# Kernel tuning notes

Measured on AMD Instinct MI355X. Metric: run time of the kernel, lower is better.

## Reference

```python
import jax, jax.numpy as jnp
import numpy as np

N, IN_DIM, HID, TASK, L = 4096, 256, 256, 128, 2
NEG_INF = -9e15


def setup_inputs() -> dict:
    key = jax.random.key(0)
    ks = jax.random.split(key, 16)
    s = 0.02
    return {
        "h": jax.random.normal(ks[0], (N, IN_DIM), jnp.float32),
        "adj": jax.random.randint(ks[1], (N, N), 0, 2, jnp.int32),
        "z": jax.random.normal(ks[2], (N, TASK), jnp.float32),
        # initial projection (in_dim -> hidden)
        "Wp": jax.random.normal(ks[3], (IN_DIM, HID), jnp.float32) * s,
        "bp": jnp.zeros((HID,), jnp.float32),
        # per-layer params, stacked over L layers
        "Wm": jax.random.normal(ks[4], (L, HID, HID), jnp.float32) * s,
        "bm": jnp.zeros((L, HID), jnp.float32),
        "Wg": jax.random.normal(ks[5], (L, HID + TASK, HID), jnp.float32) * s,
        "bg": jnp.zeros((L, HID), jnp.float32),
        "Wk": jax.random.normal(ks[6], (L, HID, HID), jnp.float32) * s,
        "bk": jnp.zeros((L, HID), jnp.float32),
        "Wq": jax.random.normal(ks[7], (L, HID, HID), jnp.float32) * s,
        "bq": jnp.zeros((L, HID), jnp.float32),
        # attention vector a: [L, 2*out_dim]; first half pairs with k, second with q
        "a": jax.random.normal(ks[8], (L, 2 * HID), jnp.float32),
    }


def reference(h, adj, z, Wp, bp, Wm, bm, Wg, bg, Wk, bk, Wq, bq, a):
    mask = adj > 0  # [N, N]
    h = h @ Wp + bp  # initial_proj -> [N, HID]
    n_layers = Wm.shape[0]
    total_gate_l1 = jnp.float32(0.0)
    for l in range(n_layers):
        raw_message = jax.nn.relu(h @ Wm[l] + bm[l])  # [N, d]
        gate = jax.nn.sigmoid(jnp.concatenate([h, z], axis=1) @ Wg[l] + bg[l])
        gated_message = gate * raw_message
        total_gate_l1 = total_gate_l1 + jnp.sum(jnp.abs(gate)) / gate.size
        q = gated_message @ Wq[l] + bq[l]  # [N, d]
        k = h @ Wk[l] + bk[l]              # [N, d]
        d = q.shape[1]
        # e[i, j] = leaky_relu([k_j, q_i] @ a) = leaky_relu(k_j . a[:d] + q_i . a[d:])
        kk = k @ a[l, :d]  # [N]
        qq = q @ a[l, d:]  # [N]
        e = jax.nn.leaky_relu(qq[:, None] + kk[None, :])  # [N, N], slope 0.01 matches torch
        attention = jax.nn.softmax(jnp.where(mask, e, NEG_INF), axis=1)
        agg_message = attention.T @ gated_message  # [N, d]
        h = (agg_message + h) / 2
    return h, total_gate_l1 / n_layers
```

## Files before the change

kernel.cpp:

```cpp
#include <hip/hip_runtime.h>
#include <hip/hip_bf16.h>
#include <stdint.h>

static constexpr int cN    = 4096;
static constexpr int cHID  = 256;
static constexpr int cTASK = 128;
static constexpr int cL    = 2;
static constexpr float RLN2 = 1.4426950408889634f;

typedef short bf16x8 __attribute__((ext_vector_type(8)));
typedef float f32x4  __attribute__((ext_vector_type(4)));

#define MFMA(a, b, c) __builtin_amdgcn_mfma_f32_16x16x32_bf16((a), (b), (c), 0, 0, 0)

static __device__ __forceinline__ uint16_t f2bf(float f) {
    uint32_t u = __float_as_uint(f);
    uint32_t r = (u + 0x7FFFu + ((u >> 16) & 1u)) >> 16;
    return (uint16_t)r;
}
static __device__ __forceinline__ float bf2f(uint16_t h) {
    return __uint_as_float(((uint32_t)h) << 16);
}
static __device__ __forceinline__ bf16x8 ld_frag(const uint16_t* p) {
    return *reinterpret_cast<const bf16x8*>(p);
}
static __device__ __forceinline__ uint32_t pkf16(float a, float b) {
    _Float16 ha = (_Float16)a, hb = (_Float16)b;
    uint16_t ua, ub;
    __builtin_memcpy(&ua, &ha, 2);
    __builtin_memcpy(&ub, &hb, 2);
    return (uint32_t)ua | ((uint32_t)ub << 16);
}
static __device__ __forceinline__ float f16lo(uint32_t v) {
    uint16_t u = (uint16_t)(v & 0xFFFFu); _Float16 h;
    __builtin_memcpy(&h, &u, 2); return (float)h;
}
static __device__ __forceinline__ float f16hi(uint32_t v) {
    uint16_t u = (uint16_t)(v >> 16); _Float16 h;
    __builtin_memcpy(&h, &u, 2); return (float)h;
}
static __device__ __forceinline__ uint32_t spread4(uint32_t x) {
    x = (x | (x << 12)) & 0x000F000Fu;
    x = (x | (x << 6))  & 0x03030303u;
    x = (x | (x << 3))  & 0x11111111u;
    return x;
}
static __device__ __forceinline__ void gload_lds16(const void* g, void* l) {
    __builtin_amdgcn_global_load_lds((const __attribute__((address_space(1))) void*)g,
                                     (__attribute__((address_space(3))) void*)l, 16, 0, 0);
}

static __device__ __forceinline__ void castT_body(const float* __restrict__ S,
                                                  uint16_t* __restrict__ D, int K, int bx,
                                                  uint16_t (*t)[72]) {
    int ntk = K / 64;
    int tk = (bx % ntk) * 64;
    int td = (bx / ntk) * 64;
    int lane = threadIdx.x & 63, w = threadIdx.x >> 6;
    for (int r = w; r < 64; r += 4) t[r][lane] = f2bf(S[(size_t)(tk + r) * 256 + td + lane]);
    __syncthreads();
    for (int r = w; r < 64; r += 4) D[(size_t)(td + r) * K + tk + lane] = t[lane][r];
}

__global__ __launch_bounds__(256) void k_prep(const float* __restrict__ h,
                                              const float* __restrict__ z,
                                              const float* __restrict__ Wp,
                                              const float* __restrict__ Wm,
                                              const float* __restrict__ Wg,
                                              const float* __restrict__ Wq,
                                              const float* __restrict__ bq,
                                              const float* __restrict__ Wk,
                                              const float* __restrict__ bk,
                                              const float* __restrict__ a,
                                              const int* __restrict__ adj,
                                              uint16_t* __restrict__ hin_bf,
                                              uint16_t* __restrict__ z_bf,
                                              uint16_t* __restrict__ WpT,
                                              uint16_t* __restrict__ WmT,
                                              uint16_t* __restrict__ WgT,
                                              float* __restrict__ wqv,
                                              float* __restrict__ wkv,
                                              float* __restrict__ cvec,
                                              uint32_t* __restrict__ maskw,
                                              float* __restrict__ gsum) {
    __shared__ uint16_t sht[64][72];
    __shared__ float shf[2][256];
    int b = blockIdx.x, tid = threadIdx.x;
    if (b == 0 && tid == 0) gsum[0] = 0.f;
    if (b < 1024) {
        int idx = b * 256 + tid;
        float4 v = reinterpret_cast<const float4*>(h)[idx];
        ushort4 o; o.x = f2bf(v.x); o.y = f2bf(v.y); o.z = f2bf(v.z); o.w = f2bf(v.w);
        reinterpret_cast<ushort4*>(hin_bf)[idx] = o;
        return;
    }
    b -= 1024;
    if (b < 512) {
        int idx = b * 256 + tid;
        float4 v = reinterpret_cast<const float4*>(z)[idx];
        ushort4 o; o.x = f2bf(v.x); o.y = f2bf(v.y); o.z = f2bf(v.z); o.w = f2bf(v.w);
        reinterpret_cast<ushort4*>(z_bf)[idx] = o;
        return;
    }
    b -= 512;
    if (b < 16) { castT_body(Wp, WpT, 256, b, sht); return; }
    b -= 16;
    if (b < 32) { castT_body(Wm + (b >> 4) * 65536, WmT + (b >> 4) * 65536, 256, b & 15, sht); return; }
    b -= 32;
    if (b < 48) { castT_body(Wg + (b / 24) * 98304, WgT + (b / 24) * 98304, 384, b % 24, sht); return; }
    b -= 48;
    if (b < 16) {
        int l = b >> 3, which = (b >> 2) & 1, q = b & 3;
        int lane = tid & 63, wid = tid >> 6;
        const float* W    = which ? (Wk + l * 65536) : (Wq + l * 65536);
        const float* avec = a + l * 512 + (which ? 0 : 256);
        float* av = shf[0];
        float* red = shf[1];
        av[tid] = avec[tid];
        __syncthreads();
        float av0 = av[lane], av1 = av[64 + lane], av2 = av[128 + lane], av3 = av[192 + lane];
        float* wv = which ? wkv : wqv;
        for (int dd = 0; dd < 16; ++dd) {
            int d = q * 64 + wid * 16 + dd;
            const float* Wr = W + (size_t)d * 256;
            float s = Wr[lane] * av0 + Wr[64 + lane] * av1 + Wr[128 + lane] * av2 + Wr[192 + lane] * av3;
            for (int off = 32; off; off >>= 1) s += __shfl_down(s, off, 64);
            if (lane == 0) wv[l * 256 + d] = s * RLN2;
        }
        if (q == 0) {
            const float* bias = which ? (bk + l * 256) : (bq + l * 256);
            red[tid] = bias[tid] * av[tid];
            __syncthreads();
            for (int off = 128; off; off >>= 1) {
                if (tid < off) red[tid] += red[tid + off];
                __syncthreads();
            }
            if (tid == 0) cvec[l * 2 + which] = red[0] * RLN2;
        }
        return;
    }
    b -= 16;
    {
        int wid = tid >> 6, lane = tid & 63;
        int i = b * 4 + wid;
        const int* row = adj + (size_t)i * cN;
        uint32_t* orow = maskw + (size_t)i * 128;
        for (int ch = 0; ch < 16; ++ch) {
            int4 v = reinterpret_cast<const int4*>(row + ch * 256)[lane];
            uint64_t b0 = __ballot(v.x > 0);
            uint64_t b1 = __ballot(v.y > 0);
            uint64_t b2 = __ballot(v.z > 0);
            uint64_t b3 = __ballot(v.w > 0);
            int k = lane & 7;
            uint32_t e0 = spread4((uint32_t)(b0 >> (8 * k)) & 0xFFu);
            uint32_t e1 = spread4((uint32_t)(b1 >> (8 * k)) & 0xFFu);
            uint32_t e2 = spread4((uint32_t)(b2 >> (8 * k)) & 0xFFu);
            uint32_t e3 = spread4((uint32_t)(b3 >> (8 * k)) & 0xFFu);
            if (lane < 8) orow[ch * 8 + k] = e0 | (e1 << 1) | (e2 << 2) | (e3 << 3);
        }
    }
}

__global__ __launch_bounds__(256) void k_pt(const uint32_t* __restrict__ maskw,
                                            uint32_t* __restrict__ maskT,
                                            const uint16_t* __restrict__ hin_bf,
                                            const uint16_t* __restrict__ WpT,
                                            const float* __restrict__ bp,
                                            float* __restrict__ h_f32,
                                            uint16_t* __restrict__ hcur_bf) {
    __shared__ uint32_t ml[256][9];
    int tid = threadIdx.x;
    if (blockIdx.x < 256) {
        int bi = blockIdx.x & 15, bj = blockIdx.x >> 4;
        int i0 = bi * 256, j0 = bj * 256;
        {
            const uint32_t* src = maskw + (size_t)(i0 + tid) * 128 + bj * 8;
            uint4 a = *reinterpret_cast<const uint4*>(src);
            uint4 b = *reinterpret_cast<const uint4*>(src + 4);
            ml[tid][0] = a.x; ml[tid][1] = a.y; ml[tid][2] = a.z; ml[tid][3] = a.w;
            ml[tid][4] = b.x; ml[tid][5] = b.y; ml[tid][6] = b.z; ml[tid][7] = b.w;
        }
        __syncthreads();
        int lane = tid & 63, wid = tid >> 6;
        int tw = wid * 2 + (lane >> 5);
        int l31 = lane & 31;
        uint32_t ow[8];
#pragma unroll
        for (int ti = 0; ti < 8; ++ti) {
            uint32_t m = ml[ti * 32 + l31][tw];
            uint32_t myw = 0;
#pragma unroll
            for (int c = 0; c < 32; ++c) {
                uint64_t bl = __ballot(((m >> c) & 1) != 0);
                uint32_t v = (lane < 32) ? (uint32_t)bl : (uint32_t)(bl >> 32);
                if (l31 == c) myw = v;
            }
            ow[ti] = myw;
        }
        uint32_t* dst = maskT + (size_t)(j0 + tw * 32 + l31) * 128 + bi * 8;
        *reinterpret_cast<uint4*>(dst)     = make_uint4(ow[0], ow[1], ow[2], ow[3]);
        *reinterpret_cast<uint4*>(dst + 4) = make_uint4(ow[4], ow[5], ow[6], ow[7]);
        return;
    }
    int bb = blockIdx.x - 256;
    int bx = bb & 63, by = bb >> 6;
    int lane = tid & 63, wid = tid >> 6;
    int wr = wid >> 1, wc = wid & 1;
    int l16 = lane & 15, g = lane >> 4;
    int i0 = bx * 64 + wr * 32, d0 = by * 64 + wc * 32;
    f32x4 acc[2][2] = {};
#pragma unroll
    for (int ks = 0; ks < 8; ++ks) {
        int kb = ks * 32 + g * 8;
        bf16x8 afr[2], bfr[2];
#pragma unroll
        for (int mr = 0; mr < 2; ++mr) afr[mr] = ld_frag(hin_bf + (size_t)(i0 + mr * 16 + l16) * 256 + kb);
#pragma unroll
        for (int nr = 0; nr < 2; ++nr) bfr[nr] = ld_frag(WpT + (size_t)(d0 + nr * 16 + l16) * 256 + kb);
#pragma unroll
        for (int mr = 0; mr < 2; ++mr)
#pragma unroll
            for (int nr = 0; nr < 2; ++nr)
                acc[mr][nr] = MFMA(afr[mr], bfr[nr], acc[mr][nr]);
    }
#pragma unroll
    for (int mr = 0; mr < 2; ++mr)
#pragma unroll
        for (int nr = 0; nr < 2; ++nr) {
            int d = d0 + nr * 16 + l16;
            float bias = bp[d];
#pragma unroll
            for (int r = 0; r < 4; ++r) {
                int i = i0 + mr * 16 + g * 4 + r;
                float v = acc[mr][nr][r] + bias;
                h_f32[(size_t)i * 256 + d] = v;
                hcur_bf[(size_t)i * 256 + d] = f2bf(v);
            }
        }
}

__global__ __launch_bounds__(256) void k_msgg(const uint16_t* __restrict__ hcur_bf,
                                              const uint16_t* __restrict__ z_bf,
                                              const uint16_t* __restrict__ WmT,
                                              const uint16_t* __restrict__ WgT,
                                              const float* __restrict__ bm,
                                              const float* __restrict__ bg,
                                              const float* __restrict__ wqv,
                                              const float* __restrict__ wkv,
                                              const float* __restrict__ cvec,
                                              uint16_t* __restrict__ gmT,
                                              float* __restrict__ qqp,
                                              float* __restrict__ kkv,
                                              float* __restrict__ gsum,
                                              int layer) {
    __shared__ float wkv_s[256], wqv_s[256];
    __shared__ float wred[4];
    int tid = threadIdx.x;
    wkv_s[tid] = wkv[layer * 256 + tid];
    wqv_s[tid] = wqv[layer * 256 + tid];
    __syncthreads();

    int bx = blockIdx.x, by = blockIdx.y;
    int lane = tid & 63, wid = tid >> 6;
    int wr = wid >> 1, wc = wid & 1;
    int l16 = lane & 15, g = lane >> 4;
    int i0 = bx * 64 + wr * 32, d0 = by * 64 + wc * 32;
    bool doKK = (by == 0);
    const uint16_t* WmTl = WmT + layer * 65536;
    const uint16_t* WgTl = WgT + layer * 98304;
    f32x4 am[2][2] = {}, ag[2][2] = {};
    float kkp[2] = {0.f, 0.f};
#pragma unroll
    for (int ks = 0; ks < 8; ++ks) {
        int kb = ks * 32 + g * 8;
        bf16x8 afr[2], bmf[2], bgf[2];
#pragma unroll
        for (int mr = 0; mr < 2; ++mr) afr[mr] = ld_frag(hcur_bf + (size_t)(i0 + mr * 16 + l16) * 256 + kb);
#pragma unroll
        for (int nr = 0; nr < 2; ++nr) {
            bmf[nr] = ld_frag(WmTl + (size_t)(d0 + nr * 16 + l16) * 256 + kb);
            bgf[nr] = ld_frag(WgTl + (size_t)(d0 + nr * 16 + l16) * 384 + kb);
        }
        if (doKK) {
#pragma unroll
            for (int mr = 0; mr < 2; ++mr)
#pragma unroll
                for (int u = 0; u < 8; ++u)
                    kkp[mr] += bf2f((uint16_t)afr[mr][u]) * wkv_s[kb + u];
        }
#pragma unroll
        for (int mr = 0; mr < 2; ++mr)
#pragma unroll
            for (int nr = 0; nr < 2; ++nr) {
                am[mr][nr] = MFMA(afr[mr], bmf[nr], am[mr][nr]);
                ag[mr][nr] = MFMA(afr[mr], bgf[nr], ag[mr][nr]);
            }
    }
#pragma unroll
    for (int ks = 0; ks < 4; ++ks) {
        int kb = ks * 32 + g * 8;
        bf16x8 afr[2], bgf[2];
#pragma unroll
        for (int mr = 0; mr < 2; ++mr) afr[mr] = ld_frag(z_bf + (size_t)(i0 + mr * 16 + l16) * 128 + kb);
#pragma unroll
        for (int nr = 0; nr < 2; ++nr) bgf[nr] = ld_frag(WgTl + (size_t)(d0 + nr * 16 + l16) * 384 + 256 + kb);
#pragma unroll
        for (int mr = 0; mr < 2; ++mr)
#pragma unroll
            for (int nr = 0; nr < 2; ++nr)
                ag[mr][nr] = MFMA(afr[mr], bgf[nr], ag[mr][nr]);
    }
    float gs = 0.f;
    float qqt[2][4] = {};
#pragma unroll
    for (int mr = 0; mr < 2; ++mr)
#pragma unroll
        for (int nr = 0; nr < 2; ++nr) {
            int d = d0 + nr * 16 + l16;
            float bmv = bm[layer * 256 + d], bgv = bg[layer * 256 + d];
            float wqd = wqv_s[d];
            ushort4 pack;
#pragma unroll
            for (int r = 0; r < 4; ++r) {
                float rm = am[mr][nr][r] + bmv; rm = rm > 0.f ? rm : 0.f;
                float gt = 1.f / (1.f + __expf(-(ag[mr][nr][r] + bgv)));
                gs += gt;
                float gmv = gt * rm;
                qqt[mr][r] += gmv * wqd;
                ((uint16_t*)&pack)[r] = f2bf(gmv);
            }
            int i = i0 + mr * 16 + g * 4;
            *reinterpret_cast<ushort4*>(gmT + (size_t)d * cN + i) = pack;
        }
#pragma unroll
    for (int mr = 0; mr < 2; ++mr)
#pragma unroll
        for (int r = 0; r < 4; ++r) {
            float v = qqt[mr][r];
            v += __shfl_xor(v, 1, 64);
            v += __shfl_xor(v, 2, 64);
            v += __shfl_xor(v, 4, 64);
            v += __shfl_xor(v, 8, 64);
            if (l16 == 0) qqp[(size_t)(by * 2 + wc) * cN + i0 + mr * 16 + g * 4 + r] = v;
        }
    if (doKK) {
        float cc = cvec[layer * 2 + 0] + cvec[layer * 2 + 1];
#pragma unroll
        for (int mr = 0; mr < 2; ++mr) {
            float v = kkp[mr];
            v += __shfl_xor(v, 16, 64);
            v += __shfl_xor(v, 32, 64);
            if (lane < 16) kkv[i0 + mr * 16 + l16] = v + cc;
        }
    }
    for (int off = 32; off; off >>= 1) gs += __shfl_down(gs, off, 64);
    if (lane == 0) wred[wid] = gs;
    __syncthreads();
    if (tid == 0) atomicAdd(gsum, wred[0] + wred[1] + wred[2] + wred[3]);
}

__global__ __launch_bounds__(256) void k_stats(const float* __restrict__ qqp,
                                               const float* __restrict__ kkv,
                                               const uint32_t* __restrict__ maskw,
                                               float2* __restrict__ stats2) {
    int wid = threadIdx.x >> 6, lane = threadIdx.x & 63;
    int i = blockIdx.x * 4 + wid;
    float qq = 0.f;
#pragma unroll
    for (int s = 0; s < 8; ++s) qq += qqp[(size_t)s * cN + i];
    const uint32_t* mrow = maskw + (size_t)i * 128;
    float den = 0.f;
#pragma unroll 4
    for (int c = 0; c < 64; ++c) {
        int j = c * 64 + lane;
        uint32_t w = mrow[j >> 5];
        bool on = (w >> (j & 31)) & 1;
        float e = qq + kkv[j];
        e = fmaxf(e, 0.01f * e);
        e = fminf(e, 80.f);
        den += on ? exp2f(e) : 0.f;
    }
#pragma unroll
    for (int off = 32; off; off >>= 1) den += __shfl_xor(den, off, 64);
    if (lane == 0) stats2[i] = make_float2(qq, den > 0.f ? 1.f / den : 0.f);
}

__global__ __launch_bounds__(512, 4) void k_agg(const uint16_t* __restrict__ gmT,
                                                const float2* __restrict__ stats2,
                                                const uint32_t* __restrict__ maskT,
                                                const float* __restrict__ kkv,
                                                uint32_t* __restrict__ part) {
    __shared__ uint16_t B_lds[2][256 * 64];
    __shared__ uint16_t A_lds[2][64 * 64];
    int jb = blockIdx.x, seg = blockIdx.y;
    int tid = threadIdx.x, lane = tid & 63, wid = tid >> 6;
    int l16 = lane & 15, g = lane >> 4;
    int jg = wid >> 2, dg = wid & 3;
    int jt = jb * 64;
    int ib0 = seg * 512;
    f32x4 acc[2][4] = {};

    int io8 = 8 * ((lane & 7) ^ (lane >> 3));
    const uint16_t* gsrc0 = gmT + (size_t)(wid * 32 + (lane >> 3)) * cN + ib0 + io8;
    auto stageB = [&](int buf, int stg) {
        const uint16_t* gs = gsrc0 + stg * 64;
        uint16_t* ldst = &B_lds[buf][(wid * 32) * 64];
#pragma unroll
        for (int c = 0; c < 4; ++c)
            gload_lds16(gs + (size_t)(c * 8) * cN, ldst + (c * 8) * 64);
    };
    int at_j = tid >> 3, at_io = tid & 7;
    float kk_t = kkv[jt + at_j];
    const uint32_t* mrow_t = maskT + (size_t)(jt + at_j) * 128;
    int ash = (at_io * 16) ^ ((at_j & 7) << 4);
    uint8_t* arow[2] = { reinterpret_cast<uint8_t*>(&A_lds[0][0]) + at_j * 128 + ash,
                         reinterpret_cast<uint8_t*>(&A_lds[1][0]) + at_j * 128 + ash };
    auto stageA = [&](int buf, int stg) {
        int ib = ib0 + stg * 64 + at_io * 8;
        uint32_t mword = mrow_t[ib >> 5];
        int shift = ib & 31;
        const float2* sp = stats2 + ib;
        union { bf16x8 v; uint16_t s[8]; } aw;
#pragma unroll
        for (int u = 0; u < 8; ++u) {
            float2 st = sp[u];
            float e = st.x + kk_t;
            e = fmaxf(e, 0.01f * e);
            e = fminf(e, 80.f);
            float w = exp2f(e) * st.y;
            aw.s[u] = ((mword >> (shift + u)) & 1) ? f2bf(w) : (uint16_t)0;
        }
        *reinterpret_cast<bf16x8*>(arow[buf]) = aw.v;
    };

    stageB(0, 0);
    stageA(0, 0);
    __syncthreads();
    int rxor = (l16 & 7) << 4;

    for (int stg = 0; stg < 8; ++stg) {
        if (stg < 7) {
            stageB((stg + 1) & 1, stg + 1);
            stageA((stg + 1) & 1, stg + 1);
        }
        const uint8_t* cb = reinterpret_cast<const uint8_t*>(&B_lds[stg & 1][0]);
        const uint8_t* ca = reinterpret_cast<const uint8_t*>(&A_lds[stg & 1][0]);
#pragma unroll
        for (int k = 0; k < 2; ++k) {
            int cofs = (k * 64 + g * 16);
            bf16x8 a0 = *reinterpret_cast<const bf16x8*>(ca + (size_t)(jg * 32 + l16) * 128 + (cofs ^ rxor));
            bf16x8 a1 = *reinterpret_cast<const bf16x8*>(ca + (size_t)(jg * 32 + 16 + l16) * 128 + (cofs ^ rxor));
            const uint8_t* bcol = cb + (size_t)(dg * 64 + l16) * 128 + (cofs ^ rxor);
#pragma unroll
            for (int nf = 0; nf < 4; ++nf) {
                bf16x8 bfr = *reinterpret_cast<const bf16x8*>(bcol + nf * (16 * 128));
                acc[0][nf] = MFMA(a0, bfr, acc[0][nf]);
                acc[1][nf] = MFMA(a1, bfr, acc[1][nf]);
            }
        }
        __syncthreads();
    }
    uint32_t* pb = part + ((size_t)(seg * 64 + jb) * 8 + wid) * 1024;
#pragma unroll
    for (int mf = 0; mf < 2; ++mf)
#pragma unroll
        for (int nf = 0; nf < 4; ++nf)
#pragma unroll
            for (int rr = 0; rr < 2; ++rr)
                pb[(((mf * 4 + nf) * 2) + rr) * 64 + lane] =
                    pkf16(acc[mf][nf][rr * 2], acc[mf][nf][rr * 2 + 1]);
}

__global__ __launch_bounds__(256) void k_resid(const uint32_t* __restrict__ part,
                                               float* __restrict__ h_f32,
                                               uint16_t* __restrict__ hcur_bf,
                                               float* __restrict__ out,
                                               const float* __restrict__ gsum,
                                               int last) {
    int jb = blockIdx.x >> 3, wid = blockIdx.x & 7;
    int tid = threadIdx.x;
    int jg = wid >> 2, dg = wid & 3;
    if (last && blockIdx.x == 0 && tid == 0)
        out[(size_t)cN * cHID] = gsum[0] * (1.f / ((float)(cN * cHID) * (float)cL));
    const uint32_t* pb = part + ((size_t)jb * 8 + wid) * 1024;
#pragma unroll
    for (int t = 0; t < 4; ++t) {
        int idx = t * 256 + tid;
        float s0 = 0.f, s1 = 0.f;
#pragma unroll
        for (int seg = 0; seg < 8; ++seg) {
            uint32_t v = pb[(size_t)seg * (64 * 8 * 1024) + idx];
            s0 += f16lo(v); s1 += f16hi(v);
        }
        int mf = idx >> 9, nf = (idx >> 7) & 3, rr = (idx >> 6) & 1, lane = idx & 63;
        int j = jb * 64 + jg * 32 + mf * 16 + (lane >> 4) * 4 + rr * 2;
        int d = dg * 64 + nf * 16 + (lane & 15);
        size_t i0 = (size_t)j * 256 + d, i1 = i0 + 256;
        float v0 = (s0 + h_f32[i0]) * 0.5f;
        float v1 = (s1 + h_f32[i1]) * 0.5f;
        if (last) {
            out[i0] = v0; out[i1] = v1;
        } else {
            h_f32[i0] = v0; h_f32[i1] = v1;
            hcur_bf[i0] = f2bf(v0); hcur_bf[i1] = f2bf(v1);
        }
    }
}

extern "C" void kernel_launch(void* const* d_in, const int* in_sizes, int n_in,
                              void* d_out, int out_size, void* d_ws, size_t ws_size,
                              hipStream_t stream) {
    const float* h   = (const float*)d_in[0];
    const int*   adj = (const int*)d_in[1];
    const float* z   = (const float*)d_in[2];
    const float* Wp  = (const float*)d_in[3];
    const float* bp  = (const float*)d_in[4];
    const float* Wm  = (const float*)d_in[5];
    const float* bm  = (const float*)d_in[6];
    const float* Wg  = (const float*)d_in[7];
    const float* bg  = (const float*)d_in[8];
    const float* Wk  = (const float*)d_in[9];
    const float* bk  = (const float*)d_in[10];
    const float* Wq  = (const float*)d_in[11];
    const float* bq  = (const float*)d_in[12];
    const float* a   = (const float*)d_in[13];
    float* out = (float*)d_out;

    uint8_t* ws = (uint8_t*)d_ws;
    size_t cur = 0;
    auto alloc = [&](size_t bytes) -> uint8_t* {
        uint8_t* p = ws + cur;
        cur = (cur + bytes + 255) & ~(size_t)255;
        return p;
    };
    uint32_t* maskw  = (uint32_t*)alloc((size_t)cN * 128 * 4);
    uint32_t* maskT  = (uint32_t*)alloc((size_t)cN * 128 * 4);
    float*    h_f32  = (float*)   alloc((size_t)cN * 256 * 4);
    uint16_t* hin_bf = (uint16_t*)alloc((size_t)cN * 256 * 2);
    uint16_t* hcur   = (uint16_t*)alloc((size_t)cN * 256 * 2);
    uint16_t* z_bf   = (uint16_t*)alloc((size_t)cN * 128 * 2);
    uint16_t* WpT    = (uint16_t*)alloc(65536 * 2);
    uint16_t* WmT    = (uint16_t*)alloc((size_t)cL * 65536 * 2);
    uint16_t* WgT    = (uint16_t*)alloc((size_t)cL * 98304 * 2);
    uint16_t* gmT    = (uint16_t*)alloc((size_t)cN * 256 * 2);
    float*    wqv    = (float*)   alloc(cL * 256 * 4);
    float*    wkv    = (float*)   alloc(cL * 256 * 4);
    float*    cvec   = (float*)   alloc(256);
    float*    qqp    = (float*)   alloc(8ull * cN * 4);
    float*    kk     = (float*)   alloc(cN * 4);
    float2*   stats2 = (float2*)  alloc(cN * 8);
    float*    gsum   = (float*)   alloc(256);
    uint32_t* part   = (uint32_t*)alloc(8ull * cN * 256 * 2);
    (void)cur;

    k_prep<<<2672, 256, 0, stream>>>(h, z, Wp, Wm, Wg, Wq, bq, Wk, bk, a, adj,
                                     hin_bf, z_bf, WpT, WmT, WgT, wqv, wkv, cvec, maskw, gsum);
    k_pt<<<512, 256, 0, stream>>>(maskw, maskT, hin_bf, WpT, bp, h_f32, hcur);

    for (int l = 0; l < cL; ++l) {
        k_msgg<<<dim3(64, 4), 256, 0, stream>>>(hcur, z_bf, WmT, WgT, bm, bg,
                                                wqv, wkv, cvec, gmT, qqp, kk, gsum, l);
        k_stats<<<cN / 4, 256, 0, stream>>>(qqp, kk, maskw, stats2);
        k_agg<<<dim3(64, 8), 512, 0, stream>>>(gmT, stats2, maskT, kk, part);
        k_resid<<<512, 256, 0, stream>>>(part, h_f32, hcur, out, gsum, l == cL - 1 ? 1 : 0);
    }
}
```

Before: 135.8 us.

## Fuse residual reduction into k_agg via last-block atomic counter

Removes the separate k_resid launch. Each k_agg block atomically increments a per-column-tile counter after writing its partials, and the last of the 8 segment blocks sums the partials and applies the residual update and output write. This saves one kernel launch per layer and its dispatch gap, at the cost of threadfences, an atomic, and serialising the reduction onto 64 blocks instead of 512.

```diff
diff --git a/kernel.cpp b/kernel.cpp
--- a/kernel.cpp
+++ b/kernel.cpp
@@ -82,11 +82,15 @@
                                               float* __restrict__ wkv,
                                               float* __restrict__ cvec,
                                               uint32_t* __restrict__ maskw,
-                                              float* __restrict__ gsum) {
+                                              float* __restrict__ gsum,
+                                              uint32_t* __restrict__ donecnt) {
     __shared__ uint16_t sht[64][72];
     __shared__ float shf[2][256];
     int b = blockIdx.x, tid = threadIdx.x;
-    if (b == 0 && tid == 0) gsum[0] = 0.f;
+    if (b == 0) {
+        if (tid == 0) gsum[0] = 0.f;
+        if (tid < 128) donecnt[tid] = 0;
+    }
     if (b < 1024) {
         int idx = b * 256 + tid;
         float4 v = reinterpret_cast<const float4*>(h)[idx];
@@ -389,7 +393,13 @@
                                                 const float2* __restrict__ stats2,
                                                 const uint32_t* __restrict__ maskT,
                                                 const float* __restrict__ kkv,
-                                                uint32_t* __restrict__ part) {
+                                                uint32_t* __restrict__ part,
+                                                float* __restrict__ h_f32,
+                                                uint16_t* __restrict__ hcur_bf,
+                                                float* __restrict__ out,
+                                                const float* __restrict__ gsum,
+                                                uint32_t* __restrict__ donecnt,
+                                                int last) {
     __shared__ uint16_t B_lds[2][256 * 64];
     __shared__ uint16_t A_lds[2][64 * 64];
     int jb = blockIdx.x, seg = blockIdx.y;
@@ -469,40 +479,43 @@
             for (int rr = 0; rr < 2; ++rr)
                 pb[(((mf * 4 + nf) * 2) + rr) * 64 + lane] =
                     pkf16(acc[mf][nf][rr * 2], acc[mf][nf][rr * 2 + 1]);
-}
-
-__global__ __launch_bounds__(256) void k_resid(const uint32_t* __restrict__ part,
-                                               float* __restrict__ h_f32,
-                                               uint16_t* __restrict__ hcur_bf,
-                                               float* __restrict__ out,
-                                               const float* __restrict__ gsum,
-                                               int last) {
-    int jb = blockIdx.x >> 3, wid = blockIdx.x & 7;
-    int tid = threadIdx.x;
-    int jg = wid >> 2, dg = wid & 3;
-    if (last && blockIdx.x == 0 && tid == 0)
+
+    __threadfence();
+    __shared__ uint32_t lastFlag;
+    if (tid == 0) {
+        uint32_t prev = atomicAdd(&donecnt[last * 64 + jb], 1u);
+        lastFlag = (prev == 7u) ? 1u : 0u;
+    }
+    __syncthreads();
+    if (!lastFlag) return;
+    __threadfence();
+    if (last && jb == 0 && tid == 0)
         out[(size_t)cN * cHID] = gsum[0] * (1.f / ((float)(cN * cHID) * (float)cL));
-    const uint32_t* pb = part + ((size_t)jb * 8 + wid) * 1024;
-#pragma unroll
-    for (int t = 0; t < 4; ++t) {
-        int idx = t * 256 + tid;
-        float s0 = 0.f, s1 = 0.f;
-#pragma unroll
-        for (int seg = 0; seg < 8; ++seg) {
-            uint32_t v = pb[(size_t)seg * (64 * 8 * 1024) + idx];
-            s0 += f16lo(v); s1 += f16hi(v);
-        }
-        int mf = idx >> 9, nf = (idx >> 7) & 3, rr = (idx >> 6) & 1, lane = idx & 63;
-        int j = jb * 64 + jg * 32 + mf * 16 + (lane >> 4) * 4 + rr * 2;
-        int d = dg * 64 + nf * 16 + (lane & 15);
-        size_t i0 = (size_t)j * 256 + d, i1 = i0 + 256;
-        float v0 = (s0 + h_f32[i0]) * 0.5f;
-        float v1 = (s1 + h_f32[i1]) * 0.5f;
-        if (last) {
-            out[i0] = v0; out[i1] = v1;
-        } else {
-            h_f32[i0] = v0; h_f32[i1] = v1;
-            hcur_bf[i0] = f2bf(v0); hcur_bf[i1] = f2bf(v1);
+#pragma unroll
+    for (int wid_r = 0; wid_r < 8; ++wid_r) {
+        int jg_r = wid_r >> 2, dg_r = wid_r & 3;
+        const uint32_t* pb2 = part + ((size_t)jb * 8 + wid_r) * 1024;
+#pragma unroll
+        for (int t = 0; t < 2; ++t) {
+            int idx = t * 512 + tid;
+            float s0 = 0.f, s1 = 0.f;
+#pragma unroll
+            for (int sg = 0; sg < 8; ++sg) {
+                uint32_t v = pb2[(size_t)sg * (64 * 8 * 1024) + idx];
+                s0 += f16lo(v); s1 += f16hi(v);
+            }
+            int mf = idx >> 9, nf = (idx >> 7) & 3, rr = (idx >> 6) & 1, ln = idx & 63;
+            int j = jb * 64 + jg_r * 32 + mf * 16 + (ln >> 4) * 4 + rr * 2;
+            int d = dg_r * 64 + nf * 16 + (ln & 15);
+            size_t p0 = (size_t)j * 256 + d, p1 = p0 + 256;
+            float v0 = (s0 + h_f32[p0]) * 0.5f;
+            float v1 = (s1 + h_f32[p1]) * 0.5f;
+            if (last) {
+                out[p0] = v0; out[p1] = v1;
+            } else {
+                h_f32[p0] = v0; h_f32[p1] = v1;
+                hcur_bf[p0] = f2bf(v0); hcur_bf[p1] = f2bf(v1);
+            }
         }
     }
 }
@@ -550,18 +563,19 @@
     float*    kk     = (float*)   alloc(cN * 4);
     float2*   stats2 = (float2*)  alloc(cN * 8);
     float*    gsum   = (float*)   alloc(256);
+    uint32_t* donecnt= (uint32_t*)alloc(128 * 4);
     uint32_t* part   = (uint32_t*)alloc(8ull * cN * 256 * 2);
     (void)cur;
 
     k_prep<<<2672, 256, 0, stream>>>(h, z, Wp, Wm, Wg, Wq, bq, Wk, bk, a, adj,
-                                     hin_bf, z_bf, WpT, WmT, WgT, wqv, wkv, cvec, maskw, gsum);
+                                     hin_bf, z_bf, WpT, WmT, WgT, wqv, wkv, cvec, maskw, gsum, donecnt);
     k_pt<<<512, 256, 0, stream>>>(maskw, maskT, hin_bf, WpT, bp, h_f32, hcur);
 
     for (int l = 0; l < cL; ++l) {
         k_msgg<<<dim3(64, 4), 256, 0, stream>>>(hcur, z_bf, WmT, WgT, bm, bg,
                                                 wqv, wkv, cvec, gmT, qqp, kk, gsum, l);
         k_stats<<<cN / 4, 256, 0, stream>>>(qqp, kk, maskw, stats2);
-        k_agg<<<dim3(64, 8), 512, 0, stream>>>(gmT, stats2, maskT, kk, part);
-        k_resid<<<512, 256, 0, stream>>>(part, h_f32, hcur, out, gsum, l == cL - 1 ? 1 : 0);
-    }
-}
+        k_agg<<<dim3(64, 8), 512, 0, stream>>>(gmT, stats2, maskT, kk, part,
+                                               h_f32, hcur, out, gsum, donecnt, l == cL - 1 ? 1 : 0);
+    }
+}
```

Result: slower. 375.0 us (+176.1%).
